# Kernel optimization log

Measured on AMD Instinct MI355X. Metric: run time of the kernel, lower is better.

## Reference

```python
import jax, jax.numpy as jnp
import numpy as np
import math

B, S, E, H = 4, 2048, 1024, 16
D = E // H
NEG_INF = -1e30  # stands in for -inf in masked_fill; softmax result identical for rows with valid entries


def setup_inputs() -> dict:
    key = jax.random.key(0)
    ks = jax.random.split(key, 7)
    sc = 1.0 / math.sqrt(E)
    return {
        "k": jax.random.normal(ks[0], (B, S, E), jnp.float32),
        "v": jax.random.normal(ks[1], (B, S, E), jnp.float32),
        "q": jax.random.normal(ks[2], (B, S, E), jnp.float32),
        "Wk": jax.random.normal(ks[3], (E, E), jnp.float32) * sc,
        "Wv": jax.random.normal(ks[4], (E, E), jnp.float32) * sc,
        "Wq": jax.random.normal(ks[5], (E, E), jnp.float32) * sc,
        "Wo": jax.random.normal(ks[6], (E, E), jnp.float32) * sc,
    }


def reference(k, v, q, Wk, Wv, Wq, Wo):
    # Linear(bias=False): y = x @ W.T
    kp = (k @ Wk.T).reshape(B, S, H, D).transpose(0, 2, 1, 3)  # [B,H,S,D]
    vp = (v @ Wv.T).reshape(B, S, H, D).transpose(0, 2, 1, 3)
    qp = (q @ Wq.T).reshape(B, S, H, D).transpose(0, 2, 1, 3)
    qp = qp / jnp.sqrt(jnp.asarray(D, qp.dtype))
    scores = jnp.einsum("bhqd,bhkd->bhqk", qp, kp)  # [B,H,S,S]
    causal = jnp.tril(jnp.ones((S, S), bool))  # [S,S]
    scores = jnp.where(causal[None, None], scores, NEG_INF)
    attn = jax.nn.softmax(scores, axis=-1)  # dropout p=0.0 (eval) -> identity
    out = jnp.einsum("bhqk,bhkd->bhqd", attn, vp)
    out = out.transpose(0, 2, 1, 3).reshape(B, S, E)
    return out @ Wo.T
```

## Files before the change

kernel.cpp:

```cpp
#include <hip/hip_runtime.h>

typedef __bf16 bf16_t;
typedef __bf16 bf16x8 __attribute__((ext_vector_type(8)));
typedef float f32x4 __attribute__((ext_vector_type(4)));


__device__ __forceinline__ void async_copy16(const void* g, void* l) {
  __builtin_amdgcn_global_load_lds(
      (const __attribute__((address_space(1))) void*)g,
      (__attribute__((address_space(3))) void*)l, 16, 0, 0);
}

__global__ void cvt_all_kernel(const float* __restrict__ q, const float* __restrict__ k,
                               const float* __restrict__ v, const float* __restrict__ wk,
                               const float* __restrict__ wv, const float* __restrict__ wq,
                               const float* __restrict__ wo, uint2* __restrict__ out) {
  constexpr int QX = 2097152, QW = 262144;
  int g = blockIdx.x * 256 + threadIdx.x;
  const float* in; int off;
  if (g < QX)               { in = q;  off = 0; }
  else if (g < 2 * QX)      { in = k;  off = QX; }
  else if (g < 3 * QX)      { in = v;  off = 2 * QX; }
  else if (g < 3 * QX + QW)     { in = wk; off = 3 * QX; }
  else if (g < 3 * QX + 2 * QW) { in = wv; off = 3 * QX + QW; }
  else if (g < 3 * QX + 3 * QW) { in = wq; off = 3 * QX + 2 * QW; }
  else                          { in = wo; off = 3 * QX + 3 * QW; }
  float4 val = ((const float4*)in)[g - off];
  union { bf16_t h[4]; uint2 u; } cv;
  cv.h[0] = (bf16_t)val.x; cv.h[1] = (bf16_t)val.y;
  cv.h[2] = (bf16_t)val.z; cv.h[3] = (bf16_t)val.w;
  out[g] = cv.u;
}

__global__ __launch_bounds__(256) void qkv_kernel(
    const bf16_t* __restrict__ qb, const bf16_t* __restrict__ kb, const bf16_t* __restrict__ vb,
    const bf16_t* __restrict__ wqb, const bf16_t* __restrict__ wkb, const bf16_t* __restrict__ wvb,
    bf16_t* __restrict__ Qp, bf16_t* __restrict__ Kp, bf16_t* __restrict__ Vt, float qscale)
{
  constexpr int K = 1024;
  __shared__ __align__(16) bf16_t As[128 * 32];
  __shared__ __align__(16) bf16_t Bs[128 * 32];
  const int tid  = threadIdx.x;
  const int lane = tid & 63;
  const int wid  = tid >> 6;
  const int quad = lane >> 4;
  const int l16  = lane & 15;
  const int bx = blockIdx.x, by = blockIdx.y;
  const int sel = by >> 3, sub = by & 7;
  const bf16_t *X, *W; bf16_t* Y; float scale = 1.0f;
  int m0, n0;
  if (sel == 0)      { X = qb;  W = wqb; Y = Qp; m0 = bx * 128; n0 = sub * 128; scale = qscale; }
  else if (sel == 1) { X = kb;  W = wkb; Y = Kp; m0 = bx * 128; n0 = sub * 128; }
  else               { X = wvb; W = vb;  Y = Vt; m0 = sub * 128; n0 = bx * 128; }
  const int wm = (wid >> 1) * 64;
  const int wn = (wid & 1) * 64;
  const int swz = quad ^ ((l16 >> 1) & 3);

  f32x4 acc[4][4] = {};

  for (int k0 = 0; k0 < K; k0 += 32) {
#pragma unroll
    for (int p = 0; p < 2; ++p) {
      int c = tid + p * 256;
      int row = c >> 2;
      int seg = ((c & 3) ^ ((c >> 3) & 3)) * 8;
      async_copy16(&X[(size_t)(m0 + row) * K + k0 + seg], (char*)As + (p * 256 + wid * 64) * 16);
      async_copy16(&W[(size_t)(n0 + row) * K + k0 + seg], (char*)Bs + (p * 256 + wid * 64) * 16);
    }
    __syncthreads();
    bf16x8 af[4], bfr[4];
#pragma unroll
    for (int i = 0; i < 4; ++i)
      af[i] = *(const bf16x8*)((const char*)As + ((wm + i * 16 + l16) * 4 + swz) * 16);
#pragma unroll
    for (int j = 0; j < 4; ++j)
      bfr[j] = *(const bf16x8*)((const char*)Bs + ((wn + j * 16 + l16) * 4 + swz) * 16);
#pragma unroll
    for (int i = 0; i < 4; ++i)
#pragma unroll
      for (int j = 0; j < 4; ++j)
        acc[i][j] = __builtin_amdgcn_mfma_f32_16x16x32_bf16(af[i], bfr[j], acc[i][j], 0, 0, 0);
    __syncthreads();
  }

#pragma unroll
  for (int i = 0; i < 4; ++i)
#pragma unroll
    for (int j = 0; j < 4; ++j)
#pragma unroll
      for (int r = 0; r < 4; ++r) {
        int row = m0 + wm + i * 16 + quad * 4 + r;
        int col = n0 + wn + j * 16 + l16;
        float val = acc[i][j][r] * scale;
        if (sel < 2) {
          int b = row >> 11, s = row & 2047;
          int h = col >> 6,  d = col & 63;
          Y[(((size_t)(b * 16 + h) << 11) + s) * 64 + d] = (bf16_t)val;
        } else {
          int h = row >> 6,  d = row & 63;
          int b = col >> 11, s = col & 2047;
          Y[(((size_t)((b * 16 + h) * 64 + d)) << 11) + s] = (bf16_t)val;
        }
      }
}

__global__ __launch_bounds__(256) void out_gemm_kernel(
    const bf16_t* __restrict__ X, const bf16_t* __restrict__ W,
    float* __restrict__ Y, int M, int N, int K)
{
  __shared__ __align__(16) bf16_t As[128 * 32];
  __shared__ __align__(16) bf16_t Bs[128 * 32];
  const int tid  = threadIdx.x;
  const int lane = tid & 63;
  const int wid  = tid >> 6;
  const int quad = lane >> 4;
  const int l16  = lane & 15;
  const int m0 = blockIdx.x * 128;
  const int n0 = blockIdx.y * 128;
  const int wm = (wid >> 1) * 64;
  const int wn = (wid & 1) * 64;
  const int swz = quad ^ ((l16 >> 1) & 3);

  f32x4 acc[4][4] = {};

  for (int k0 = 0; k0 < K; k0 += 32) {
#pragma unroll
    for (int p = 0; p < 2; ++p) {
      int c = tid + p * 256;
      int row = c >> 2;
      int seg = ((c & 3) ^ ((c >> 3) & 3)) * 8;
      async_copy16(&X[(size_t)(m0 + row) * K + k0 + seg], (char*)As + (p * 256 + wid * 64) * 16);
      async_copy16(&W[(size_t)(n0 + row) * K + k0 + seg], (char*)Bs + (p * 256 + wid * 64) * 16);
    }
    __syncthreads();
    bf16x8 af[4], bfr[4];
#pragma unroll
    for (int i = 0; i < 4; ++i)
      af[i] = *(const bf16x8*)((const char*)As + ((wm + i * 16 + l16) * 4 + swz) * 16);
#pragma unroll
    for (int j = 0; j < 4; ++j)
      bfr[j] = *(const bf16x8*)((const char*)Bs + ((wn + j * 16 + l16) * 4 + swz) * 16);
#pragma unroll
    for (int i = 0; i < 4; ++i)
#pragma unroll
      for (int j = 0; j < 4; ++j)
        acc[i][j] = __builtin_amdgcn_mfma_f32_16x16x32_bf16(af[i], bfr[j], acc[i][j], 0, 0, 0);
    __syncthreads();
  }

#pragma unroll
  for (int i = 0; i < 4; ++i)
#pragma unroll
    for (int j = 0; j < 4; ++j)
#pragma unroll
      for (int r = 0; r < 4; ++r) {
        int row = m0 + wm + i * 16 + quad * 4 + r;
        int col = n0 + wn + j * 16 + l16;
        Y[(size_t)row * N + col] = acc[i][j][r];
      }
}

__global__ __launch_bounds__(256, 2) void attn_kernel(
    const bf16_t* __restrict__ Qp, const bf16_t* __restrict__ Kp,
    const bf16_t* __restrict__ Vt, bf16_t* __restrict__ O)
{
  constexpr int S = 2048, D = 64, E = 1024;
  constexpr int BQ = 128, BK = 128, PST = 136;
  __shared__ __align__(16) bf16_t Ks[BK * D];
  __shared__ __align__(16) bf16_t Vs[D * BK];
  __shared__ __align__(16) bf16_t Ps[BQ * PST];

  const int tid = threadIdx.x, lane = tid & 63, wid = tid >> 6;
  const int quad = lane >> 4, l16 = lane & 15;
  const int bh = blockIdx.y;
  const int b = bh >> 4, h = bh & 15;
  const int qt = gridDim.x - 1 - blockIdx.x;
  const int q0 = qt * BQ;
  const size_t base  = (size_t)bh * S * D;
  const size_t baseV = (size_t)bh * D * S;
  const int qrow = wid * 32;

  bf16x8 qf[2][2];
#pragma unroll
  for (int rt = 0; rt < 2; ++rt)
#pragma unroll
    for (int kk = 0; kk < 2; ++kk)
      qf[rt][kk] = *(const bf16x8*)(&Qp[base + (size_t)(q0 + qrow + rt * 16 + l16) * D + kk * 32 + quad * 8]);

#pragma unroll
  for (int p = 0; p < 4; ++p) {
    int c = tid + p * 256;
    int gk = c ^ ((c >> 3) & 7);
    async_copy16(&Kp[base + (size_t)(gk >> 3) * D + (gk & 7) * 8],
                 (char*)Ks + (p * 256 + wid * 64) * 16);
    int gv = c ^ ((c >> 4) & 7);
    async_copy16(&Vt[baseV + (size_t)(gv >> 4) * S + (gv & 15) * 8],
                 (char*)Vs + (p * 256 + wid * 64) * 16);
  }
  __syncthreads();

  f32x4 o_acc[2][4] = {};
  f32x4 o_sum[2] = {};
  bf16x8 ones;
#pragma unroll
  for (int e = 0; e < 8; ++e) ones[e] = (bf16_t)1.0f;

  const int nkt = qt + 1;
  for (int kt = 0; kt < nkt; ++kt) {
    const bool diag = (kt == nkt - 1);
    const int jlim0 = diag ? 2 * wid     : 7;
    const int jlim1 = diag ? 2 * wid + 1 : 7;
    const int kklim = diag ? wid : 3;
    f32x4 sc[2][8] = {};
#pragma unroll
    for (int kk = 0; kk < 2; ++kk)
#pragma unroll
      for (int j = 0; j < 8; ++j)
        if (j <= jlim1) {
          int L = (j * 16 + l16) * 8 + kk * 4 + quad;
          bf16x8 bk = *(const bf16x8*)(&Ks[(L ^ (l16 & 7)) * 8]);
          if (j <= jlim0)
            sc[0][j] = __builtin_amdgcn_mfma_f32_16x16x32_bf16(qf[0][kk], bk, sc[0][j], 0, 0, 0);
          sc[1][j] = __builtin_amdgcn_mfma_f32_16x16x32_bf16(qf[1][kk], bk, sc[1][j], 0, 0, 0);
        }
    if (diag) {
#pragma unroll
      for (int rt = 0; rt < 2; ++rt)
#pragma unroll
        for (int j = 0; j < 8; ++j)
#pragma unroll
          for (int r = 0; r < 4; ++r)
            if (j * 16 + l16 > qrow + rt * 16 + quad * 4 + r) sc[rt][j][r] = -1e30f;
    }
#pragma unroll
    for (int rt = 0; rt < 2; ++rt) {
      const int jlive = rt ? jlim1 : jlim0;
#pragma unroll
      for (int j = 0; j < 8; ++j)
        if (j <= jlim1) {
          int kcol = j * 16 + l16;
#pragma unroll
          for (int r = 0; r < 4; ++r) {
            float pp = (j <= jlive) ? __builtin_amdgcn_exp2f(sc[rt][j][r]) : 0.0f;
            Ps[(qrow + rt * 16 + quad * 4 + r) * PST + kcol] = (bf16_t)pp;
          }
        }
    }
    __syncthreads();
    if (kt + 1 < nkt) {
      const int k0n = (kt + 1) * BK;
#pragma unroll
      for (int p = 0; p < 4; ++p) {
        int c = tid + p * 256;
        int gk = c ^ ((c >> 3) & 7);
        async_copy16(&Kp[base + (size_t)(k0n + (gk >> 3)) * D + (gk & 7) * 8],
                     (char*)Ks + (p * 256 + wid * 64) * 16);
      }
    }
#pragma unroll
    for (int kk = 0; kk < 4; ++kk)
      if (kk <= kklim) {
        bf16x8 ap0 = *(const bf16x8*)(&Ps[(qrow + l16) * PST + kk * 32 + quad * 8]);
        bf16x8 ap1 = *(const bf16x8*)(&Ps[(qrow + 16 + l16) * PST + kk * 32 + quad * 8]);
#pragma unroll
        for (int t = 0; t < 4; ++t) {
          int L = (t * 16 + l16) * 16 + kk * 4 + quad;
          bf16x8 bv = *(const bf16x8*)(&Vs[(L ^ (l16 & 7)) * 8]);
          o_acc[0][t] = __builtin_amdgcn_mfma_f32_16x16x32_bf16(ap0, bv, o_acc[0][t], 0, 0, 0);
          o_acc[1][t] = __builtin_amdgcn_mfma_f32_16x16x32_bf16(ap1, bv, o_acc[1][t], 0, 0, 0);
        }
        o_sum[0] = __builtin_amdgcn_mfma_f32_16x16x32_bf16(ap0, ones, o_sum[0], 0, 0, 0);
        o_sum[1] = __builtin_amdgcn_mfma_f32_16x16x32_bf16(ap1, ones, o_sum[1], 0, 0, 0);
      }
    __syncthreads();
    if (kt + 1 < nkt) {
      const int k0n = (kt + 1) * BK;
#pragma unroll
      for (int p = 0; p < 4; ++p) {
        int c = tid + p * 256;
        int gv = c ^ ((c >> 4) & 7);
        async_copy16(&Vt[baseV + (size_t)(gv >> 4) * S + k0n + (gv & 15) * 8],
                     (char*)Vs + (p * 256 + wid * 64) * 16);
      }
      __syncthreads();
    }
  }

#pragma unroll
  for (int rt = 0; rt < 2; ++rt)
#pragma unroll
    for (int t = 0; t < 4; ++t)
#pragma unroll
      for (int r = 0; r < 4; ++r) {
        int row = q0 + qrow + rt * 16 + quad * 4 + r;
        int d = t * 16 + l16;
        float val = o_acc[rt][t][r] / o_sum[rt][r];
        O[((size_t)(b * S + row)) * E + h * D + d] = (bf16_t)val;
      }
}

extern "C" void kernel_launch(void* const* d_in, const int* in_sizes, int n_in,
                              void* d_out, int out_size, void* d_ws, size_t ws_size,
                              hipStream_t stream) {
  const float* k_in = (const float*)d_in[0];
  const float* v_in = (const float*)d_in[1];
  const float* q_in = (const float*)d_in[2];
  const float* Wk_in = (const float*)d_in[3];
  const float* Wv_in = (const float*)d_in[4];
  const float* Wq_in = (const float*)d_in[5];
  const float* Wo_in = (const float*)d_in[6];
  float* out = (float*)d_out;

  constexpr int    M = 8192, N = 1024, K = 1024;
  constexpr size_t SZ_X = (size_t)M * K * 2;
  constexpr size_t SZ_W = (size_t)N * K * 2;

  char* ws = (char*)d_ws;
  bf16_t* qb  = (bf16_t*)(ws);
  bf16_t* kb  = (bf16_t*)(ws + SZ_X);
  bf16_t* vb  = (bf16_t*)(ws + 2 * SZ_X);
  bf16_t* wkb = (bf16_t*)(ws + 3 * SZ_X);
  bf16_t* wvb = (bf16_t*)(ws + 3 * SZ_X + SZ_W);
  bf16_t* wqb = (bf16_t*)(ws + 3 * SZ_X + 2 * SZ_W);
  bf16_t* wob = (bf16_t*)(ws + 3 * SZ_X + 3 * SZ_W);
  bf16_t* Qp  = (bf16_t*)(ws + 3 * SZ_X + 4 * SZ_W);
  bf16_t* Kp  = (bf16_t*)(ws + 4 * SZ_X + 4 * SZ_W);
  bf16_t* Vtg = (bf16_t*)(ws + 5 * SZ_X + 4 * SZ_W);
  bf16_t* Ob  = qb;

  cvt_all_kernel<<<28672, 256, 0, stream>>>(q_in, k_in, v_in, Wk_in, Wv_in, Wq_in, Wo_in,
                                            (uint2*)ws);

  qkv_kernel<<<dim3(64, 24), 256, 0, stream>>>(qb, kb, vb, wqb, wkb, wvb,
                                               Qp, Kp, Vtg, 0.125f * 1.44269504f);

  attn_kernel<<<dim3(2048 / 128, 4 * 16), 256, 0, stream>>>(Qp, Kp, Vtg, Ob);

  out_gemm_kernel<<<dim3(M / 128, N / 128), 256, 0, stream>>>(Ob, wob, out, M, N, K);
}
```

Before: 337.3 us.

## Rewrite attention inner loop with 32x32 MFMA, register-resident P, and double-buffered K/V

The attention kernel moves from 16x16x32 to 32x32x16 MFMAs and computes S^T so the exp'd probabilities stay in registers. They are packed to bf16 and rearranged with permlane32 swaps instead of being round-tripped through a shared-memory P tile. K/V tiles shrink to 64 keys and are double-buffered, so the next tile's async load overlaps compute with one barrier per iteration, and occupancy is raised to 3 blocks/CU. Row sums are accumulated in registers instead of via an extra ones-MFMA. The trade-offs are more loop iterations, inline asm that depends on gfx950 instructions, and higher register pressure.

```diff
diff --git a/kernel.cpp b/kernel.cpp
--- a/kernel.cpp
+++ b/kernel.cpp
@@ -3,12 +3,19 @@
 typedef __bf16 bf16_t;
 typedef __bf16 bf16x8 __attribute__((ext_vector_type(8)));
 typedef float f32x4 __attribute__((ext_vector_type(4)));
+typedef float f32x16 __attribute__((ext_vector_type(16)));
 
 
 __device__ __forceinline__ void async_copy16(const void* g, void* l) {
   __builtin_amdgcn_global_load_lds(
       (const __attribute__((address_space(1))) void*)g,
       (__attribute__((address_space(3))) void*)l, 16, 0, 0);
+}
+
+__device__ __forceinline__ unsigned pk_bf16(float lo, float hi) {
+  unsigned r;
+  asm("v_cvt_pk_bf16_f32 %0, %1, %2" : "=v"(r) : "v"(lo), "v"(hi));
+  return r;
 }
 
 __global__ void cvt_all_kernel(const float* __restrict__ q, const float* __restrict__ k,
@@ -160,143 +167,162 @@
       }
 }
 
-__global__ __launch_bounds__(256, 2) void attn_kernel(
+__global__ __launch_bounds__(256, 3) void attn_kernel(
     const bf16_t* __restrict__ Qp, const bf16_t* __restrict__ Kp,
     const bf16_t* __restrict__ Vt, bf16_t* __restrict__ O)
 {
   constexpr int S = 2048, D = 64, E = 1024;
-  constexpr int BQ = 128, BK = 128, PST = 136;
-  __shared__ __align__(16) bf16_t Ks[BK * D];
-  __shared__ __align__(16) bf16_t Vs[D * BK];
-  __shared__ __align__(16) bf16_t Ps[BQ * PST];
+  constexpr int BQ = 128, BK = 64;
+  __shared__ __align__(16) bf16_t Ks[2][8 * 64 * 8];
+  __shared__ __align__(16) bf16_t Vs[2][8 * 64 * 8];
+  __shared__ float rsbuf[128];
 
   const int tid = threadIdx.x, lane = tid & 63, wid = tid >> 6;
-  const int quad = lane >> 4, l16 = lane & 15;
+  const int l31 = lane & 31, hi = lane >> 5;
   const int bh = blockIdx.y;
   const int b = bh >> 4, h = bh & 15;
-  const int qt = gridDim.x - 1 - blockIdx.x;
+  const int qt = (int)gridDim.x - 1 - (int)blockIdx.x;
   const int q0 = qt * BQ;
   const size_t base  = (size_t)bh * S * D;
   const size_t baseV = (size_t)bh * D * S;
-  const int qrow = wid * 32;
-
-  bf16x8 qf[2][2];
-#pragma unroll
-  for (int rt = 0; rt < 2; ++rt)
-#pragma unroll
-    for (int kk = 0; kk < 2; ++kk)
-      qf[rt][kk] = *(const bf16x8*)(&Qp[base + (size_t)(q0 + qrow + rt * 16 + l16) * D + kk * 32 + quad * 8]);
-
-#pragma unroll
-  for (int p = 0; p < 4; ++p) {
-    int c = tid + p * 256;
-    int gk = c ^ ((c >> 3) & 7);
-    async_copy16(&Kp[base + (size_t)(gk >> 3) * D + (gk & 7) * 8],
-                 (char*)Ks + (p * 256 + wid * 64) * 16);
-    int gv = c ^ ((c >> 4) & 7);
-    async_copy16(&Vt[baseV + (size_t)(gv >> 4) * S + (gv & 15) * 8],
-                 (char*)Vs + (p * 256 + wid * 64) * 16);
+  const int qmin = q0 + wid * 32;
+  const int qmax = qmin + 31;
+
+  bf16x8 qf[4];
+#pragma unroll
+  for (int ks = 0; ks < 4; ++ks)
+    qf[ks] = *(const bf16x8*)&Qp[base + (size_t)(qmin + l31) * D + ks * 16 + hi * 8];
+
+#pragma unroll
+  for (int is = 0; is < 2; ++is) {
+    const int c = is * 256 + tid;
+    const int p = c >> 6, row = c & 63;
+    async_copy16(&Kp[base + (size_t)row * D + p * 8],
+                 (char*)Ks[0] + (is * 256 + wid * 64) * 16);
+    async_copy16(&Vt[baseV + (size_t)row * S + p * 8],
+                 (char*)Vs[0] + (is * 256 + wid * 64) * 16);
   }
   __syncthreads();
 
-  f32x4 o_acc[2][4] = {};
-  f32x4 o_sum[2] = {};
-  bf16x8 ones;
-#pragma unroll
-  for (int e = 0; e < 8; ++e) ones[e] = (bf16_t)1.0f;
-
-  const int nkt = qt + 1;
-  for (int kt = 0; kt < nkt; ++kt) {
-    const bool diag = (kt == nkt - 1);
-    const int jlim0 = diag ? 2 * wid     : 7;
-    const int jlim1 = diag ? 2 * wid + 1 : 7;
-    const int kklim = diag ? wid : 3;
-    f32x4 sc[2][8] = {};
-#pragma unroll
-    for (int kk = 0; kk < 2; ++kk)
-#pragma unroll
-      for (int j = 0; j < 8; ++j)
-        if (j <= jlim1) {
-          int L = (j * 16 + l16) * 8 + kk * 4 + quad;
-          bf16x8 bk = *(const bf16x8*)(&Ks[(L ^ (l16 & 7)) * 8]);
-          if (j <= jlim0)
-            sc[0][j] = __builtin_amdgcn_mfma_f32_16x16x32_bf16(qf[0][kk], bk, sc[0][j], 0, 0, 0);
-          sc[1][j] = __builtin_amdgcn_mfma_f32_16x16x32_bf16(qf[1][kk], bk, sc[1][j], 0, 0, 0);
+  const f32x16 z16 = {};
+  f32x16 oa0 = {}, oa1 = {};
+  float rs = 0.0f;
+  const int nks = 2 * qt + 2;
+
+  for (int kt = 0; kt < nks; ++kt) {
+    const int cur = kt & 1;
+    const int k0 = kt * BK;
+    if (kt + 1 < nks) {
+      const int k0n = k0 + BK;
+#pragma unroll
+      for (int is = 0; is < 2; ++is) {
+        const int c = is * 256 + tid;
+        const int p = c >> 6, row = c & 63;
+        async_copy16(&Kp[base + (size_t)(k0n + row) * D + p * 8],
+                     (char*)Ks[cur ^ 1] + (is * 256 + wid * 64) * 16);
+        async_copy16(&Vt[baseV + (size_t)row * S + k0n + p * 8],
+                     (char*)Vs[cur ^ 1] + (is * 256 + wid * 64) * 16);
+      }
+    }
+    if (k0 <= qmax) {
+      const bf16_t* ksb = Ks[cur];
+      const bf16_t* vsb = Vs[cur];
+      f32x16 sc0, sc1;
+      {
+        const bf16x8 kf0 = *(const bf16x8*)&ksb[(hi * 64 + l31) * 8];
+        const bf16x8 kf1 = *(const bf16x8*)&ksb[(hi * 64 + 32 + l31) * 8];
+        sc0 = __builtin_amdgcn_mfma_f32_32x32x16_bf16(kf0, qf[0], z16, 0, 0, 0);
+        sc1 = __builtin_amdgcn_mfma_f32_32x32x16_bf16(kf1, qf[0], z16, 0, 0, 0);
+      }
+#pragma unroll
+      for (int ks = 1; ks < 4; ++ks) {
+        const bf16x8 kf0 = *(const bf16x8*)&ksb[((ks * 2 + hi) * 64 + l31) * 8];
+        const bf16x8 kf1 = *(const bf16x8*)&ksb[((ks * 2 + hi) * 64 + 32 + l31) * 8];
+        sc0 = __builtin_amdgcn_mfma_f32_32x32x16_bf16(kf0, qf[ks], sc0, 0, 0, 0);
+        sc1 = __builtin_amdgcn_mfma_f32_32x32x16_bf16(kf1, qf[ks], sc1, 0, 0, 0);
+      }
+      if (k0 + 63 > qmin) {
+        const int qg = qmin + l31;
+#pragma unroll
+        for (int r = 0; r < 16; ++r) {
+          const int kg = k0 + (r & 3) + 8 * (r >> 2) + 4 * hi;
+          if (kg > qg)      sc0[r] = -1e30f;
+          if (kg + 32 > qg) sc1[r] = -1e30f;
         }
-    if (diag) {
-#pragma unroll
-      for (int rt = 0; rt < 2; ++rt)
-#pragma unroll
-        for (int j = 0; j < 8; ++j)
-#pragma unroll
-          for (int r = 0; r < 4; ++r)
-            if (j * 16 + l16 > qrow + rt * 16 + quad * 4 + r) sc[rt][j][r] = -1e30f;
-    }
-#pragma unroll
-    for (int rt = 0; rt < 2; ++rt) {
-      const int jlive = rt ? jlim1 : jlim0;
-#pragma unroll
-      for (int j = 0; j < 8; ++j)
-        if (j <= jlim1) {
-          int kcol = j * 16 + l16;
-#pragma unroll
-          for (int r = 0; r < 4; ++r) {
-            float pp = (j <= jlive) ? __builtin_amdgcn_exp2f(sc[rt][j][r]) : 0.0f;
-            Ps[(qrow + rt * 16 + quad * 4 + r) * PST + kcol] = (bf16_t)pp;
-          }
+      }
+#pragma unroll
+      for (int r = 0; r < 16; ++r) {
+        sc0[r] = __builtin_amdgcn_exp2f(sc0[r]);
+        sc1[r] = __builtin_amdgcn_exp2f(sc1[r]);
+      }
+      {
+        float s0 = 0.f, s1 = 0.f, s2 = 0.f, s3 = 0.f;
+#pragma unroll
+        for (int r = 0; r < 16; r += 4) {
+          s0 += sc0[r]     + sc1[r];
+          s1 += sc0[r + 1] + sc1[r + 1];
+          s2 += sc0[r + 2] + sc1[r + 2];
+          s3 += sc0[r + 3] + sc1[r + 3];
+        }
+        rs += (s0 + s1) + (s2 + s3);
+      }
+      unsigned pw[16];
+      {
+        unsigned a0 = pk_bf16(sc0[0], sc0[1]),   a1 = pk_bf16(sc0[2], sc0[3]);
+        unsigned b0 = pk_bf16(sc0[4], sc0[5]),   b1 = pk_bf16(sc0[6], sc0[7]);
+        unsigned c0 = pk_bf16(sc0[8], sc0[9]),   c1 = pk_bf16(sc0[10], sc0[11]);
+        unsigned d0 = pk_bf16(sc0[12], sc0[13]), d1 = pk_bf16(sc0[14], sc0[15]);
+        asm("v_permlane32_swap_b32 %0, %1" : "+v"(a0), "+v"(b0));
+        asm("v_permlane32_swap_b32 %0, %1" : "+v"(a1), "+v"(b1));
+        asm("v_permlane32_swap_b32 %0, %1" : "+v"(c0), "+v"(d0));
+        asm("v_permlane32_swap_b32 %0, %1" : "+v"(c1), "+v"(d1));
+        pw[0] = a0; pw[1] = a1; pw[2] = b0; pw[3] = b1;
+        pw[4] = c0; pw[5] = c1; pw[6] = d0; pw[7] = d1;
+      }
+      {
+        unsigned a0 = pk_bf16(sc1[0], sc1[1]),   a1 = pk_bf16(sc1[2], sc1[3]);
+        unsigned b0 = pk_bf16(sc1[4], sc1[5]),   b1 = pk_bf16(sc1[6], sc1[7]);
+        unsigned c0 = pk_bf16(sc1[8], sc1[9]),   c1 = pk_bf16(sc1[10], sc1[11]);
+        unsigned d0 = pk_bf16(sc1[12], sc1[13]), d1 = pk_bf16(sc1[14], sc1[15]);
+        asm("v_permlane32_swap_b32 %0, %1" : "+v"(a0), "+v"(b0));
+        asm("v_permlane32_swap_b32 %0, %1" : "+v"(a1), "+v"(b1));
+        asm("v_permlane32_swap_b32 %0, %1" : "+v"(c0), "+v"(d0));
+        asm("v_permlane32_swap_b32 %0, %1" : "+v"(c1), "+v"(d1));
+        pw[8]  = a0; pw[9]  = a1; pw[10] = b0; pw[11] = b1;
+        pw[12] = c0; pw[13] = c1; pw[14] = d0; pw[15] = d1;
+      }
+      union U8 { unsigned u[4]; bf16x8 v; };
+#pragma unroll
+      for (int kb = 0; kb < 2; ++kb)
+#pragma unroll
+        for (int ks2 = 0; ks2 < 2; ++ks2) {
+          U8 pu;
+          pu.u[0] = pw[kb * 8 + ks2 * 4 + 0];
+          pu.u[1] = pw[kb * 8 + ks2 * 4 + 1];
+          pu.u[2] = pw[kb * 8 + ks2 * 4 + 2];
+          pu.u[3] = pw[kb * 8 + ks2 * 4 + 3];
+          const int pnl = kb * 4 + ks2 * 2 + hi;
+          const bf16x8 vf0 = *(const bf16x8*)&vsb[(pnl * 64 + l31) * 8];
+          const bf16x8 vf1 = *(const bf16x8*)&vsb[(pnl * 64 + 32 + l31) * 8];
+          oa0 = __builtin_amdgcn_mfma_f32_32x32x16_bf16(pu.v, vf0, oa0, 0, 0, 0);
+          oa1 = __builtin_amdgcn_mfma_f32_32x32x16_bf16(pu.v, vf1, oa1, 0, 0, 0);
         }
     }
     __syncthreads();
-    if (kt + 1 < nkt) {
-      const int k0n = (kt + 1) * BK;
-#pragma unroll
-      for (int p = 0; p < 4; ++p) {
-        int c = tid + p * 256;
-        int gk = c ^ ((c >> 3) & 7);
-        async_copy16(&Kp[base + (size_t)(k0n + (gk >> 3)) * D + (gk & 7) * 8],
-                     (char*)Ks + (p * 256 + wid * 64) * 16);
-      }
-    }
-#pragma unroll
-    for (int kk = 0; kk < 4; ++kk)
-      if (kk <= kklim) {
-        bf16x8 ap0 = *(const bf16x8*)(&Ps[(qrow + l16) * PST + kk * 32 + quad * 8]);
-        bf16x8 ap1 = *(const bf16x8*)(&Ps[(qrow + 16 + l16) * PST + kk * 32 + quad * 8]);
-#pragma unroll
-        for (int t = 0; t < 4; ++t) {
-          int L = (t * 16 + l16) * 16 + kk * 4 + quad;
-          bf16x8 bv = *(const bf16x8*)(&Vs[(L ^ (l16 & 7)) * 8]);
-          o_acc[0][t] = __builtin_amdgcn_mfma_f32_16x16x32_bf16(ap0, bv, o_acc[0][t], 0, 0, 0);
-          o_acc[1][t] = __builtin_amdgcn_mfma_f32_16x16x32_bf16(ap1, bv, o_acc[1][t], 0, 0, 0);
-        }
-        o_sum[0] = __builtin_amdgcn_mfma_f32_16x16x32_bf16(ap0, ones, o_sum[0], 0, 0, 0);
-        o_sum[1] = __builtin_amdgcn_mfma_f32_16x16x32_bf16(ap1, ones, o_sum[1], 0, 0, 0);
-      }
-    __syncthreads();
-    if (kt + 1 < nkt) {
-      const int k0n = (kt + 1) * BK;
-#pragma unroll
-      for (int p = 0; p < 4; ++p) {
-        int c = tid + p * 256;
-        int gv = c ^ ((c >> 4) & 7);
-        async_copy16(&Vt[baseV + (size_t)(gv >> 4) * S + k0n + (gv & 15) * 8],
-                     (char*)Vs + (p * 256 + wid * 64) * 16);
-      }
-      __syncthreads();
-    }
-  }
-
-#pragma unroll
-  for (int rt = 0; rt < 2; ++rt)
-#pragma unroll
-    for (int t = 0; t < 4; ++t)
-#pragma unroll
-      for (int r = 0; r < 4; ++r) {
-        int row = q0 + qrow + rt * 16 + quad * 4 + r;
-        int d = t * 16 + l16;
-        float val = o_acc[rt][t][r] / o_sum[rt][r];
-        O[((size_t)(b * S + row)) * E + h * D + d] = (bf16_t)val;
-      }
+  }
+
+  const float full = rs + __shfl(rs, lane ^ 32);
+  if (lane < 32) rsbuf[wid * 32 + l31] = full;
+  __syncthreads();
+#pragma unroll
+  for (int r = 0; r < 16; ++r) {
+    const int crow = (r & 3) + 8 * (r >> 2) + 4 * hi;
+    const float inv = __builtin_amdgcn_rcpf(rsbuf[wid * 32 + crow]);
+    const int row = q0 + wid * 32 + crow;
+    const size_t rowoff = ((size_t)(b * S + row)) * E + h * D;
+    O[rowoff + l31]      = (bf16_t)(oa0[r] * inv);
+    O[rowoff + 32 + l31] = (bf16_t)(oa1[r] * inv);
+  }
 }
 
 extern "C" void kernel_launch(void* const* d_in, const int* in_sizes, int n_in,
```

Measured after the change: 323.4 us. -4.1%, faster.
